# Kernel tuning notes

Measured on AMD Instinct MI355X. Metric: run time of the kernel, lower is better.

## Reference

```python
import jax, jax.numpy as jnp
import numpy as np

DIM = 1024
HEADS = 16
SEEDS = 1
EPS = 1e-5

def _ln(x, g, b):
    mu = jnp.mean(x, axis=-1, keepdims=True)
    var = jnp.mean((x - mu) ** 2, axis=-1, keepdims=True)
    return (x - mu) * jax.lax.rsqrt(var + EPS) * g + b

def setup_inputs() -> dict:
    key = jax.random.key(0)
    ks = jax.random.split(key, 12)
    B, N = 32, 2048
    X = jax.random.normal(ks[0], (B, N, DIM), dtype=jnp.float32)
    mask = jax.random.randint(ks[1], (B, N), 0, 2, dtype=jnp.int32)
    s = 0.02
    return {
        "X": X,
        "mask": mask,
        "S": jax.random.normal(ks[2], (1, SEEDS, DIM), dtype=jnp.float32) * s,
        "Wq": jax.random.normal(ks[3], (DIM, DIM), dtype=jnp.float32) * s,
        "bq": jnp.zeros((DIM,), jnp.float32),
        "Wk": jax.random.normal(ks[4], (DIM, DIM), dtype=jnp.float32) * s,
        "bk": jnp.zeros((DIM,), jnp.float32),
        "Wv": jax.random.normal(ks[5], (DIM, DIM), dtype=jnp.float32) * s,
        "bv": jnp.zeros((DIM,), jnp.float32),
        "Wo": jax.random.normal(ks[6], (DIM, DIM), dtype=jnp.float32) * s,
        "bo": jnp.zeros((DIM,), jnp.float32),
        "g0": jnp.ones((DIM,), jnp.float32),
        "b0": jnp.zeros((DIM,), jnp.float32),
        "g1": jnp.ones((DIM,), jnp.float32),
        "b1": jnp.zeros((DIM,), jnp.float32),
    }

def reference(X, mask, S, Wq, bq, Wk, bk, Wv, bv, Wo, bo, g0, b0, g1, b1):
    B, N, _ = X.shape
    dh = DIM // HEADS
    Q = jnp.broadcast_to(S, (B, SEEDS, DIM))             # [B,S,D]
    Qp = (Q @ Wq.T + bq).reshape(B, SEEDS, HEADS, dh)    # split along channel dim == torch split/cat
    Kp = (X @ Wk.T + bk).reshape(B, N, HEADS, dh)
    Vp = (X @ Wv.T + bv).reshape(B, N, HEADS, dh)
    # NB: original scales by sqrt(dim_V), not sqrt(head_dim)
    score = jnp.einsum('bshd,bnhd->bhsn', Qp, Kp) / jnp.sqrt(jnp.float32(DIM))
    m = mask[:, None, None, :]                           # [B,1,1,N]
    score = jnp.where(m == 0, jnp.float32(-1e12), score)
    A = jax.nn.softmax(score, axis=-1) * m
    O = jnp.einsum('bhsn,bnhd->bshd', A, Vp).reshape(B, SEEDS, DIM)
    O = Q + O
    O = _ln(O, g0, b0)
    O = O + jax.nn.relu(O @ Wo.T + bo)
    O = _ln(O, g1, b1)
    return O[:, 0, :]  # num_seeds == 1 -> squeeze
```

## Files before the change

### kernel.cpp

```cpp
#include <hip/hip_runtime.h>
#include <hip/hip_bf16.h>
#include <cstdint>

#define DIM   1024
#define HEADS 16
#define BB    32
#define NN    2048
#define DH    64
#define PARTS 8
#define TS    32

constexpr float SCALE = 0.03125f;
constexpr float LN_EPS = 1e-5f;

typedef __attribute__((ext_vector_type(8))) short short8v;
typedef __attribute__((ext_vector_type(4))) short short4v;
typedef __attribute__((ext_vector_type(4))) float f32x4;

__device__ __forceinline__ short f2bf(float f) {
  union { __hip_bfloat16 h; short s; } u;
  u.h = __float2bfloat16(f);
  return u.s;
}
__device__ __forceinline__ float bf2f(short s) {
  union { unsigned int i; float f; } u;
  u.i = ((unsigned int)(unsigned short)s) << 16;
  return u.f;
}
__device__ __forceinline__ short8v pack8(float4 a, float4 b) {
  short8v v;
  v[0] = f2bf(a.x); v[1] = f2bf(a.y); v[2] = f2bf(a.z); v[3] = f2bf(a.w);
  v[4] = f2bf(b.x); v[5] = f2bf(b.y); v[6] = f2bf(b.z); v[7] = f2bf(b.w);
  return v;
}

__device__ __forceinline__ float block_sum256(float v, volatile float* red) {
  #pragma unroll
  for (int off = 32; off; off >>= 1) v += __shfl_xor(v, off);
  __syncthreads();
  if ((threadIdx.x & 63) == 0) red[threadIdx.x >> 6] = v;
  __syncthreads();
  return red[0] + red[1] + red[2] + red[3];
}

__global__ void k_front1(const int* __restrict__ mask, const float* __restrict__ S,
                         const float* __restrict__ Wq, const float* __restrict__ bq,
                         float* __restrict__ Qp, int* __restrict__ idx,
                         int* __restrict__ cnt) {
  __shared__ int wsum[4];
  int tid = threadIdx.x;
  if (blockIdx.x < 32) {
    int b = blockIdx.x;
    const int* mb = mask + b * NN;
    int base = tid * 8;
    int loc[8], c = 0;
    #pragma unroll
    for (int i = 0; i < 8; ++i) { loc[i] = mb[base + i]; c += (loc[i] != 0); }
    int pre = c;
    #pragma unroll
    for (int off = 1; off < 64; off <<= 1) {
      int y = __shfl_up(pre, off);
      if ((tid & 63) >= off) pre += y;
    }
    if ((tid & 63) == 63) wsum[tid >> 6] = pre;
    __syncthreads();
    int wo = 0;
    for (int wv = 0; wv < (tid >> 6); ++wv) wo += wsum[wv];
    int pos = wo + pre - c;
    int* ib = idx + b * NN;
    #pragma unroll
    for (int i = 0; i < 8; ++i) if (loc[i]) ib[pos++] = base + i;
    if (tid == 255) cnt[b] = wo + pre;
    return;
  }
  int q = blockIdx.x - 32;
  int rgrp = tid >> 5, l32 = tid & 31;
  int d = q * 8 + rgrp;
  const float* wr = Wq + (size_t)d * DIM + l32 * 4;
  const float* sp = S + l32 * 4;
  float a = 0.f;
  #pragma unroll
  for (int k = 0; k < 8; ++k) {
    float4 av = *(const float4*)(wr + k * 128);
    float4 sv = *(const float4*)(sp + k * 128);
    a += av.x * sv.x + av.y * sv.y + av.z * sv.z + av.w * sv.w;
  }
  #pragma unroll
  for (int off = 16; off; off >>= 1) a += __shfl_xor(a, off);
  if (l32 == 0) Qp[d] = a + bq[d];
}

__global__ void k_front2(const float* __restrict__ Qp, const float* __restrict__ Wk,
                         const float* __restrict__ bk, short* __restrict__ qk_bf,
                         float* __restrict__ qb) {
  __shared__ float qpl[DH];
  int tid = threadIdx.x;
  int h = blockIdx.x >> 2, cblk = blockIdx.x & 3;
  if (tid < DH) qpl[tid] = Qp[h * DH + tid];
  __syncthreads();
  if (cblk == 0 && tid < 64) {
    float v = qpl[tid] * bk[h * DH + tid];
    #pragma unroll
    for (int off = 32; off; off >>= 1) v += __shfl_xor(v, off);
    if (tid == 0) qb[h] = v;
  }
  int c = cblk * 256 + tid;
  float acc = 0.f;
  #pragma unroll 8
  for (int d0 = 0; d0 < DH; ++d0)
    acc += qpl[d0] * Wk[(size_t)(h * DH + d0) * DIM + c];
  int slot = (c >> 3) ^ (h & 7);
  qk_bf[h * 1024 + slot * 8 + (c & 7)] = f2bf(acc);
}

#define LOADSET(pfA_, pfB_, tt)                                            \
  { int tbL = pstart + (tt) * TS;                                          \
    _Pragma("unroll")                                                      \
    for (int k = 0; k < 8; ++k) {                                          \
      int i = tid + k * 512;                                               \
      int row = i >> 7, c8 = i & 127;                                      \
      int sl = tbL + row; if (sl >= pend) sl = pend - 1;                   \
      int n = ib[sl];                                                      \
      const float4* xg = (const float4*)(Xb + (size_t)n * DIM + c8 * 8);   \
      pfA_[k] = xg[0]; pfB_[k] = xg[1];                                    \
    } }

#define WRITESET(pfA_, pfB_)                                               \
  { _Pragma("unroll")                                                      \
    for (int k = 0; k < 8; ++k) {                                          \
      int i = tid + k * 512;                                               \
      int row = i >> 7, c8 = i & 127;                                      \
      int sw = c8 ^ (row & 7) ^ ((row >> 3) << 3);                         \
      *(short8v*)(xlds + row * 1024 + sw * 8) = pack8(pfA_[k], pfB_[k]);   \
    } }

__global__ __launch_bounds__(512, 1) void k_fused8(const float* __restrict__ X,
                                                   const short* __restrict__ qk_bf,
                                                   const float* __restrict__ qb,
                                                   const int* __restrict__ idx,
                                                   const int* __restrict__ cnt,
                                                   short* __restrict__ Zt,
                                                   float* __restrict__ lt_g) {
  __shared__ short qlds[HEADS * 1024];
  __shared__ short xlds[TS * 1024];
  __shared__ __align__(16) short elbf[HEADS * 40];
  __shared__ __align__(16) short zst[HEADS * 1040];
  __shared__ float lt_l[32];
  int tid = threadIdx.x;
  int b = blockIdx.x >> 3, p = blockIdx.x & 7;
  int count = cnt[b];
  int chunk = (count + PARTS - 1) / PARTS;
  int pstart = p * chunk;
  int pend = pstart + chunk; if (pend > count) pend = count;
  int len = pend - pstart;
  int ntsub = (len + TS - 1) / TS;
  {
    const short8v* qg = (const short8v*)qk_bf;
    short8v* ql = (short8v*)qlds;
    #pragma unroll
    for (int i = 0; i < 4; ++i) ql[tid + i * 512] = qg[tid + i * 512];
  }
  int wv = tid >> 6, lane = tid & 63;
  int r16 = lane & 15, kg = lane >> 4;
  int hx = r16 & 7;
  const int* ib = idx + b * NN;
  const float* Xb = X + (size_t)b * NN * DIM;
  const short* qrow = qlds + r16 * 1024;
  float qbv = qb[r16];
  int srow = wv * 16 + r16;
  int axor = (srow & 7) ^ (((srow >> 3) & 3) << 3);
  f32x4 acc[8];
  #pragma unroll
  for (int blk = 0; blk < 8; ++blk) acc[blk] = (f32x4){0.f, 0.f, 0.f, 0.f};
  float lrun_reg = 0.f;
  float4 pfA[8], pfB[8];
  if (ntsub > 0) LOADSET(pfA, pfB, 0)
  __syncthreads();

  for (int t = 0; t < ntsub; ++t) {
    int tb = pstart + t * TS;
    __syncthreads();
    WRITESET(pfA, pfB)
    __syncthreads();
    if (t + 1 < ntsub) LOADSET(pfA, pfB, t + 1)
    if (wv < 2) {
      const short* arow = xlds + srow * 1024;
      f32x4 qa = {0.f, 0.f, 0.f, 0.f};
      #pragma unroll 8
      for (int m = 0; m < 32; ++m) {
        int c8 = 4 * m + kg;
        short8v af = *(const short8v*)(arow + ((c8 ^ axor) << 3));
        short8v bf = *(const short8v*)(qrow + ((c8 ^ hx) << 3));
        qa = __builtin_amdgcn_mfma_f32_16x16x32_bf16(af, bf, qa, 0, 0, 0);
      }
      float es = 0.f;
      #pragma unroll
      for (int j = 0; j < 4; ++j) {
        int slot = tb + wv * 16 + kg * 4 + j;
        float e = (slot < pend) ? __expf((qa[j] + qbv) * SCALE) : 0.f;
        elbf[r16 * 40 + (wv * 16 + kg * 4 + j)] = f2bf(e);
        es += e;
      }
      es += __shfl_xor(es, 16);
      es += __shfl_xor(es, 32);
      if (kg == 0) lt_l[wv * 16 + r16] = es;
    }
    __syncthreads();
    {
      int g = kg;
      short8v ea = *(const short8v*)(elbf + r16 * 40 + g * 8);
      #pragma unroll
      for (int blk = 0; blk < 8; ++blk) {
        int c = wv * 128 + blk * 16 + r16;
        int ch = c >> 3, cl = c & 7;
        short8v xb;
        #pragma unroll
        for (int u = 0; u < 8; ++u) {
          int s = g * 8 + u;
          int sw = ch ^ (s & 7) ^ ((s >> 3) << 3);
          xb[u] = xlds[s * 1024 + sw * 8 + cl];
        }
        acc[blk] = __builtin_amdgcn_mfma_f32_16x16x32_bf16(ea, xb, acc[blk], 0, 0, 0);
      }
      if (tid < 16) lrun_reg += lt_l[tid] + lt_l[16 + tid];
    }
  }
  if (tid < 16) lt_g[(b * PARTS + p) * HEADS + tid] = lrun_reg;
  #pragma unroll
  for (int blk = 0; blk < 8; ++blk) {
    int c = wv * 128 + blk * 16 + r16;
    #pragma unroll
    for (int j = 0; j < 4; ++j)
      zst[(kg * 4 + j) * 1040 + c] = f2bf(acc[blk][j]);
  }
  __syncthreads();
  short* zbase = Zt + ((size_t)(b * PARTS + p) * HEADS) * DIM;
  #pragma unroll
  for (int it = 0; it < 8; ++it) {
    int e4 = it * 2048 + tid * 4;
    int h = e4 >> 10, c = e4 & 1023;
    *(short4v*)(zbase + h * DIM + c) = *(const short4v*)(zst + h * 1040 + c);
  }
}

__global__ __launch_bounds__(256) void k_tov3(const short* __restrict__ Zt,
                                              const float* __restrict__ lt_g,
                                              const float* __restrict__ Wv,
                                              float* __restrict__ T,
                                              float* __restrict__ lsum) {
  int b = blockIdx.x >> 4, h = blockIdx.x & 15;
  int tid = threadIdx.x;
  __shared__ float zlds[DIM];
  float L = 0.f;
  #pragma unroll
  for (int t = 0; t < PARTS; ++t) L += lt_g[(b * PARTS + t) * HEADS + h];
  float inv = L > 0.f ? 1.f / L : 0.f;
  float4 zs = make_float4(0.f, 0.f, 0.f, 0.f);
  #pragma unroll
  for (int t = 0; t < PARTS; ++t) {
    short4v z4 = *(const short4v*)(Zt + ((size_t)(b * PARTS + t) * HEADS + h) * DIM + tid * 4);
    zs.x += bf2f(z4[0]); zs.y += bf2f(z4[1]);
    zs.z += bf2f(z4[2]); zs.w += bf2f(z4[3]);
  }
  zs.x *= inv; zs.y *= inv; zs.z *= inv; zs.w *= inv;
  *(float4*)(zlds + tid * 4) = zs;
  __syncthreads();
  int wv = tid >> 6, lane = tid & 63;
  float4 zr[4];
  #pragma unroll
  for (int j = 0; j < 4; ++j) zr[j] = *(const float4*)(zlds + lane * 4 + j * 256);
  for (int i = 0; i < 16; ++i) {
    int df = h * 64 + wv * 16 + i;
    const float* wr = Wv + (size_t)df * DIM + lane * 4;
    float a = 0.f;
    #pragma unroll
    for (int j = 0; j < 4; ++j) {
      float4 w4 = *(const float4*)(wr + j * 256);
      a += zr[j].x * w4.x + zr[j].y * w4.y + zr[j].z * w4.z + zr[j].w * w4.w;
    }
    #pragma unroll
    for (int off = 32; off; off >>= 1) a += __shfl_xor(a, off);
    if (lane == 0) T[(size_t)b * DIM + df] = a;
  }
  if (tid == 0) lsum[b * HEADS + h] = L > 0.f ? 1.f : 0.f;
}

__global__ void k_ln0(const float* __restrict__ S, const float* __restrict__ T,
                      const float* __restrict__ lsum, const float* __restrict__ bv,
                      const float* __restrict__ g0, const float* __restrict__ b0,
                      float* __restrict__ U) {
  __shared__ float red[4];
  int b = blockIdx.x, tid = threadIdx.x, d0 = tid * 4;
  float4 s4 = *(const float4*)(S + d0);
  float4 t4 = *(const float4*)(T + (size_t)b * DIM + d0);
  float4 v4 = *(const float4*)(bv + d0);
  float lh = lsum[b * HEADS + (d0 >> 6)];
  float x0 = s4.x + t4.x + lh * v4.x;
  float x1 = s4.y + t4.y + lh * v4.y;
  float x2 = s4.z + t4.z + lh * v4.z;
  float x3 = s4.w + t4.w + lh * v4.w;
  float mu = block_sum256(x0 + x1 + x2 + x3, red) * (1.f / DIM);
  float e0 = x0 - mu, e1 = x1 - mu, e2 = x2 - mu, e3 = x3 - mu;
  float var = block_sum256(e0 * e0 + e1 * e1 + e2 * e2 + e3 * e3, red) * (1.f / DIM);
  float r = rsqrtf(var + LN_EPS);
  float4 g4 = *(const float4*)(g0 + d0);
  float4 bb4 = *(const float4*)(b0 + d0);
  float4 o;
  o.x = e0 * r * g4.x + bb4.x;
  o.y = e1 * r * g4.y + bb4.y;
  o.z = e2 * r * g4.z + bb4.z;
  o.w = e3 * r * g4.w + bb4.w;
  *(float4*)(U + (size_t)b * DIM + d0) = o;
}

__global__ void k_wo(const float* __restrict__ U, const float* __restrict__ Wo,
                     const float* __restrict__ bo, float* __restrict__ R) {
  int wave = threadIdx.x >> 6, lane = threadIdx.x & 63;
  int dfb = blockIdx.x;
  for (int dot = wave; dot < 128; dot += 4) {
    int b = dot >> 2, dfl = dot & 3;
    int df = dfb * 4 + dfl;
    const float* wr = Wo + (size_t)df * DIM + lane * 4;
    const float* ur = U + (size_t)b * DIM + lane * 4;
    float acc = 0.f;
    #pragma unroll
    for (int k = 0; k < 4; ++k) {
      float4 a = *(const float4*)(wr + k * 256);
      float4 u = *(const float4*)(ur + k * 256);
      acc += a.x * u.x + a.y * u.y + a.z * u.z + a.w * u.w;
    }
    #pragma unroll
    for (int off = 32; off; off >>= 1) acc += __shfl_xor(acc, off);
    if (lane == 0) R[(size_t)b * DIM + df] = fmaxf(acc + bo[df], 0.f);
  }
}

__global__ void k_ln1(const float* __restrict__ U, const float* __restrict__ R,
                      const float* __restrict__ g1, const float* __restrict__ b1,
                      float* __restrict__ out) {
  __shared__ float red[4];
  int b = blockIdx.x, tid = threadIdx.x, d0 = tid * 4;
  float4 u4 = *(const float4*)(U + (size_t)b * DIM + d0);
  float4 r4 = *(const float4*)(R + (size_t)b * DIM + d0);
  float x0 = u4.x + r4.x, x1 = u4.y + r4.y, x2 = u4.z + r4.z, x3 = u4.w + r4.w;
  float mu = block_sum256(x0 + x1 + x2 + x3, red) * (1.f / DIM);
  float e0 = x0 - mu, e1 = x1 - mu, e2 = x2 - mu, e3 = x3 - mu;
  float var = block_sum256(e0 * e0 + e1 * e1 + e2 * e2 + e3 * e3, red) * (1.f / DIM);
  float r = rsqrtf(var + LN_EPS);
  float4 g4 = *(const float4*)(g1 + d0);
  float4 bb4 = *(const float4*)(b1 + d0);
  float4 o;
  o.x = e0 * r * g4.x + bb4.x;
  o.y = e1 * r * g4.y + bb4.y;
  o.z = e2 * r * g4.z + bb4.z;
  o.w = e3 * r * g4.w + bb4.w;
  *(float4*)(out + (size_t)b * DIM + d0) = o;
}

extern "C" void kernel_launch(void* const* d_in, const int* in_sizes, int n_in,
                              void* d_out, int out_size, void* d_ws, size_t ws_size,
                              hipStream_t stream) {
  (void)in_sizes; (void)n_in; (void)out_size; (void)ws_size;
  const float* X  = (const float*)d_in[0];
  const int*   mask = (const int*)d_in[1];
  const float* S  = (const float*)d_in[2];
  const float* Wq = (const float*)d_in[3];
  const float* bq = (const float*)d_in[4];
  const float* Wk = (const float*)d_in[5];
  const float* bk = (const float*)d_in[6];
  const float* Wv = (const float*)d_in[7];
  const float* bv = (const float*)d_in[8];
  const float* Wo = (const float*)d_in[9];
  const float* bo = (const float*)d_in[10];
  const float* g0 = (const float*)d_in[11];
  const float* b0 = (const float*)d_in[12];
  const float* g1 = (const float*)d_in[13];
  const float* b1 = (const float*)d_in[14];
  float* out = (float*)d_out;

  char* base  = (char*)d_ws;
  size_t off = 0;
  short* Zt   = (short*)(base + off); off += (size_t)BB * PARTS * HEADS * DIM * 2;
  short* qkbf = (short*)(base + off); off += HEADS * 1024 * 2;
  float* qb   = (float*)(base + off); off += 64;
  float* lt   = (float*)(base + off); off += (size_t)BB * PARTS * HEADS * 4;
  float* lsum = (float*)(base + off); off += BB * HEADS * 4;
  int*   idx  = (int*)(base + off);   off += (size_t)BB * NN * 4;
  int*   cnt  = (int*)(base + off);   off += 256;
  float* Qp   = (float*)(base + off); off += DIM * 4;
  float* T    = (float*)(base + off); off += (size_t)BB * DIM * 4;
  float* U    = (float*)(base + off); off += (size_t)BB * DIM * 4;
  float* R    = (float*)(base + off); off += (size_t)BB * DIM * 4;

  k_front1 <<<160, 256, 0, stream>>>(mask, S, Wq, bq, Qp, idx, cnt);
  k_front2 <<<64,  256, 0, stream>>>(Qp, Wk, bk, qkbf, qb);
  k_fused8 <<<256, 512, 0, stream>>>(X, qkbf, qb, idx, cnt, Zt, lt);
  k_tov3   <<<512, 256, 0, stream>>>(Zt, lt, Wv, T, lsum);
  k_ln0    <<<32,  256, 0, stream>>>(S, T, lsum, bv, g0, b0, U);
  k_wo     <<<256, 256, 0, stream>>>(U, Wo, bo, R);
  k_ln1    <<<32,  256, 0, stream>>>(U, R, g1, b1, out);
}
```

Before: 81.03 us.

## Split attention over more partitions, store partials in fragment layout, read Q from global

Doubles the per-batch partition count so the fused attention kernel launches twice as many blocks across the GPU's CUs, and halves the register prefetch buffer by loading tiles in two 16-row halves. It drops the LDS copy of the query matrix, reading it straight from global/cache instead. It also writes the partial Z accumulators directly in MFMA fragment order as packed bf16 pairs, with no LDS staging pass, and adapts the reduction kernel to that layout. The cost is more partial results to reduce and less overlap between loads and compute, since the second half is loaded synchronously.

After: 114.8 us. +41.6%, slower.

```diff
diff --git a/kernel.cpp b/kernel.cpp
--- a/kernel.cpp
+++ b/kernel.cpp
@@ -7,7 +7,7 @@
 #define BB    32
 #define NN    2048
 #define DH    64
-#define PARTS 8
+#define PARTS 16
 #define TS    32
 
 constexpr float SCALE = 0.03125f;
@@ -22,9 +22,9 @@
   u.h = __float2bfloat16(f);
   return u.s;
 }
-__device__ __forceinline__ float bf2f(short s) {
+__device__ __forceinline__ float bf2f(unsigned short s) {
   union { unsigned int i; float f; } u;
-  u.i = ((unsigned int)(unsigned short)s) << 16;
+  u.i = ((unsigned int)s) << 16;
   return u.f;
 }
 __device__ __forceinline__ short8v pack8(float4 a, float4 b) {
@@ -32,6 +32,10 @@
   v[0] = f2bf(a.x); v[1] = f2bf(a.y); v[2] = f2bf(a.z); v[3] = f2bf(a.w);
   v[4] = f2bf(b.x); v[5] = f2bf(b.y); v[6] = f2bf(b.z); v[7] = f2bf(b.w);
   return v;
+}
+__device__ __forceinline__ unsigned int packpair(float a, float b) {
+  return (unsigned int)(unsigned short)f2bf(a) |
+         ((unsigned int)(unsigned short)f2bf(b) << 16);
 }
 
 __device__ __forceinline__ float block_sum256(float v, volatile float* red) {
@@ -113,59 +117,53 @@
   qk_bf[h * 1024 + slot * 8 + (c & 7)] = f2bf(acc);
 }
 
-#define LOADSET(pfA_, pfB_, tt)                                            \
-  { int tbL = pstart + (tt) * TS;                                          \
+#define LOADH(pf_, tt, half_)                                              \
+  { int tbL = pstart + (tt) * TS + (half_) * 16;                           \
     _Pragma("unroll")                                                      \
-    for (int k = 0; k < 8; ++k) {                                          \
+    for (int k = 0; k < 4; ++k) {                                          \
       int i = tid + k * 512;                                               \
-      int row = i >> 7, c8 = i & 127;                                      \
-      int sl = tbL + row; if (sl >= pend) sl = pend - 1;                   \
+      int row16 = i >> 7, c8 = i & 127;                                    \
+      int sl = tbL + row16; if (sl >= pend) sl = pend - 1;                 \
       int n = ib[sl];                                                      \
       const float4* xg = (const float4*)(Xb + (size_t)n * DIM + c8 * 8);   \
-      pfA_[k] = xg[0]; pfB_[k] = xg[1];                                    \
+      pf_[k].a = xg[0]; pf_[k].b = xg[1];                                  \
     } }
 
-#define WRITESET(pfA_, pfB_)                                               \
+#define WRITEH(pf_, half_)                                                 \
   { _Pragma("unroll")                                                      \
-    for (int k = 0; k < 8; ++k) {                                          \
+    for (int k = 0; k < 4; ++k) {                                          \
       int i = tid + k * 512;                                               \
-      int row = i >> 7, c8 = i & 127;                                      \
+      int row = (half_) * 16 + (i >> 7), c8 = i & 127;                     \
       int sw = c8 ^ (row & 7) ^ ((row >> 3) << 3);                         \
-      *(short8v*)(xlds + row * 1024 + sw * 8) = pack8(pfA_[k], pfB_[k]);   \
+      *(short8v*)(xlds + row * 1024 + sw * 8) = pack8(pf_[k].a, pf_[k].b); \
     } }
 
-__global__ __launch_bounds__(512, 1) void k_fused8(const float* __restrict__ X,
-                                                   const short* __restrict__ qk_bf,
-                                                   const float* __restrict__ qb,
-                                                   const int* __restrict__ idx,
-                                                   const int* __restrict__ cnt,
-                                                   short* __restrict__ Zt,
-                                                   float* __restrict__ lt_g) {
-  __shared__ short qlds[HEADS * 1024];
+struct pfpair { float4 a, b; };
+
+__global__ __launch_bounds__(512, 1) void k_fused10(const float* __restrict__ X,
+                                                    const short* __restrict__ qk_bf,
+                                                    const float* __restrict__ qb,
+                                                    const int* __restrict__ idx,
+                                                    const int* __restrict__ cnt,
+                                                    unsigned int* __restrict__ Zt32,
+                                                    float* __restrict__ lt_g) {
   __shared__ short xlds[TS * 1024];
   __shared__ __align__(16) short elbf[HEADS * 40];
-  __shared__ __align__(16) short zst[HEADS * 1040];
   __shared__ float lt_l[32];
   int tid = threadIdx.x;
-  int b = blockIdx.x >> 3, p = blockIdx.x & 7;
+  int b = blockIdx.x >> 4, p = blockIdx.x & 15;
   int count = cnt[b];
   int chunk = (count + PARTS - 1) / PARTS;
   int pstart = p * chunk;
   int pend = pstart + chunk; if (pend > count) pend = count;
   int len = pend - pstart;
-  int ntsub = (len + TS - 1) / TS;
-  {
-    const short8v* qg = (const short8v*)qk_bf;
-    short8v* ql = (short8v*)qlds;
-    #pragma unroll
-    for (int i = 0; i < 4; ++i) ql[tid + i * 512] = qg[tid + i * 512];
-  }
+  int ntsub = len > 0 ? (len + TS - 1) / TS : 0;
   int wv = tid >> 6, lane = tid & 63;
   int r16 = lane & 15, kg = lane >> 4;
   int hx = r16 & 7;
   const int* ib = idx + b * NN;
   const float* Xb = X + (size_t)b * NN * DIM;
-  const short* qrow = qlds + r16 * 1024;
+  const short* qrow = qk_bf + r16 * 1024;
   float qbv = qb[r16];
   int srow = wv * 16 + r16;
   int axor = (srow & 7) ^ (((srow >> 3) & 3) << 3);
@@ -173,16 +171,17 @@
   #pragma unroll
   for (int blk = 0; blk < 8; ++blk) acc[blk] = (f32x4){0.f, 0.f, 0.f, 0.f};
   float lrun_reg = 0.f;
-  float4 pfA[8], pfB[8];
-  if (ntsub > 0) LOADSET(pfA, pfB, 0)
-  __syncthreads();
+  pfpair pf[4];
+  if (ntsub > 0) LOADH(pf, 0, 0)
 
   for (int t = 0; t < ntsub; ++t) {
     int tb = pstart + t * TS;
     __syncthreads();
-    WRITESET(pfA, pfB)
+    WRITEH(pf, 0)
+    LOADH(pf, t, 1)
+    WRITEH(pf, 1)
+    if (t + 1 < ntsub) LOADH(pf, t + 1, 0)
     __syncthreads();
-    if (t + 1 < ntsub) LOADSET(pfA, pfB, t + 1)
     if (wv < 2) {
       const short* arow = xlds + srow * 1024;
       f32x4 qa = {0.f, 0.f, 0.f, 0.f};
@@ -207,8 +206,7 @@
     }
     __syncthreads();
     {
-      int g = kg;
-      short8v ea = *(const short8v*)(elbf + r16 * 40 + g * 8);
+      short8v ea = *(const short8v*)(elbf + r16 * 40 + kg * 8);
       #pragma unroll
       for (int blk = 0; blk < 8; ++blk) {
         int c = wv * 128 + blk * 16 + r16;
@@ -216,7 +214,7 @@
         short8v xb;
         #pragma unroll
         for (int u = 0; u < 8; ++u) {
-          int s = g * 8 + u;
+          int s = kg * 8 + u;
           int sw = ch ^ (s & 7) ^ ((s >> 3) << 3);
           xb[u] = xlds[s * 1024 + sw * 8 + cl];
         }
@@ -226,24 +224,16 @@
     }
   }
   if (tid < 16) lt_g[(b * PARTS + p) * HEADS + tid] = lrun_reg;
+  unsigned int* Zp = Zt32 + (size_t)(b * PARTS + p) * 8192;
   #pragma unroll
   for (int blk = 0; blk < 8; ++blk) {
-    int c = wv * 128 + blk * 16 + r16;
-    #pragma unroll
-    for (int j = 0; j < 4; ++j)
-      zst[(kg * 4 + j) * 1040 + c] = f2bf(acc[blk][j]);
-  }
-  __syncthreads();
-  short* zbase = Zt + ((size_t)(b * PARTS + p) * HEADS) * DIM;
-  #pragma unroll
-  for (int it = 0; it < 8; ++it) {
-    int e4 = it * 2048 + tid * 4;
-    int h = e4 >> 10, c = e4 & 1023;
-    *(short4v*)(zbase + h * DIM + c) = *(const short4v*)(zst + h * 1040 + c);
-  }
-}
-
-__global__ __launch_bounds__(256) void k_tov3(const short* __restrict__ Zt,
+    #pragma unroll
+    for (int jp = 0; jp < 2; ++jp)
+      Zp[(blk * 2 + jp) * 512 + tid] = packpair(acc[blk][2 * jp], acc[blk][2 * jp + 1]);
+  }
+}
+
+__global__ __launch_bounds__(256) void k_tov4(const unsigned int* __restrict__ Zt32,
                                               const float* __restrict__ lt_g,
                                               const float* __restrict__ Wv,
                                               float* __restrict__ T,
@@ -255,28 +245,34 @@
   #pragma unroll
   for (int t = 0; t < PARTS; ++t) L += lt_g[(b * PARTS + t) * HEADS + h];
   float inv = L > 0.f ? 1.f / L : 0.f;
+  int kg = h >> 2, j = h & 3, jp = j >> 1, hi = j & 1;
+  int c4 = tid * 4;
+  int wvq = c4 >> 7, blk = (c4 >> 4) & 7, r16 = c4 & 15;
+  size_t zoff = (size_t)(blk * 2 + jp) * 512 + wvq * 64 + kg * 16 + r16;
   float4 zs = make_float4(0.f, 0.f, 0.f, 0.f);
   #pragma unroll
   for (int t = 0; t < PARTS; ++t) {
-    short4v z4 = *(const short4v*)(Zt + ((size_t)(b * PARTS + t) * HEADS + h) * DIM + tid * 4);
-    zs.x += bf2f(z4[0]); zs.y += bf2f(z4[1]);
-    zs.z += bf2f(z4[2]); zs.w += bf2f(z4[3]);
+    const unsigned int* zp = Zt32 + (size_t)(b * PARTS + t) * 8192 + zoff;
+    unsigned int u0 = zp[0], u1 = zp[1], u2 = zp[2], u3 = zp[3];
+    if (hi) { u0 >>= 16; u1 >>= 16; u2 >>= 16; u3 >>= 16; }
+    zs.x += bf2f((unsigned short)u0); zs.y += bf2f((unsigned short)u1);
+    zs.z += bf2f((unsigned short)u2); zs.w += bf2f((unsigned short)u3);
   }
   zs.x *= inv; zs.y *= inv; zs.z *= inv; zs.w *= inv;
-  *(float4*)(zlds + tid * 4) = zs;
+  *(float4*)(zlds + c4) = zs;
   __syncthreads();
   int wv = tid >> 6, lane = tid & 63;
   float4 zr[4];
   #pragma unroll
-  for (int j = 0; j < 4; ++j) zr[j] = *(const float4*)(zlds + lane * 4 + j * 256);
+  for (int jj = 0; jj < 4; ++jj) zr[jj] = *(const float4*)(zlds + lane * 4 + jj * 256);
   for (int i = 0; i < 16; ++i) {
     int df = h * 64 + wv * 16 + i;
     const float* wr = Wv + (size_t)df * DIM + lane * 4;
     float a = 0.f;
     #pragma unroll
-    for (int j = 0; j < 4; ++j) {
-      float4 w4 = *(const float4*)(wr + j * 256);
-      a += zr[j].x * w4.x + zr[j].y * w4.y + zr[j].z * w4.z + zr[j].w * w4.w;
+    for (int jj = 0; jj < 4; ++jj) {
+      float4 w4 = *(const float4*)(wr + jj * 256);
+      a += zr[jj].x * w4.x + zr[jj].y * w4.y + zr[jj].z * w4.z + zr[jj].w * w4.w;
     }
     #pragma unroll
     for (int off = 32; off; off >>= 1) a += __shfl_xor(a, off);
@@ -380,7 +376,8 @@
 
   char* base  = (char*)d_ws;
   size_t off = 0;
-  short* Zt   = (short*)(base + off); off += (size_t)BB * PARTS * HEADS * DIM * 2;
+  unsigned int* Zt32 = (unsigned int*)(base + off);
+  off += (size_t)BB * PARTS * 8192 * 4;
   short* qkbf = (short*)(base + off); off += HEADS * 1024 * 2;
   float* qb   = (float*)(base + off); off += 64;
   float* lt   = (float*)(base + off); off += (size_t)BB * PARTS * HEADS * 4;
@@ -394,8 +391,8 @@
 
   k_front1 <<<160, 256, 0, stream>>>(mask, S, Wq, bq, Qp, idx, cnt);
   k_front2 <<<64,  256, 0, stream>>>(Qp, Wk, bk, qkbf, qb);
-  k_fused8 <<<256, 512, 0, stream>>>(X, qkbf, qb, idx, cnt, Zt, lt);
-  k_tov3   <<<512, 256, 0, stream>>>(Zt, lt, Wv, T, lsum);
+  k_fused10<<<512, 512, 0, stream>>>(X, qkbf, qb, idx, cnt, Zt32, lt);
+  k_tov4   <<<512, 256, 0, stream>>>(Zt32, lt, Wv, T, lsum);
   k_ln0    <<<32,  256, 0, stream>>>(S, T, lsum, bv, g0, b0, U);
   k_wo     <<<256, 256, 0, stream>>>(U, Wo, bo, R);
   k_ln1    <<<32,  256, 0, stream>>>(U, R, g1, b1, out);
```
